# Optimization experiments

Measured on AMD Instinct MI355X. Metric: run time of the kernel, lower is better.

## Reference

```python
import jax, jax.numpy as jnp
import numpy as np
import math

D_MODEL = 512
N_HEADS = 2
B, S = 2, 1024
THRESHOLD = 0.5  # kwargs default 'sparsity_threshold'


def setup_inputs() -> dict:
    key = jax.random.key(0)
    ks = jax.random.split(key, 10)
    D, H = D_MODEL, D_MODEL // 4
    std = 0.02
    return {
        "x": jax.random.normal(ks[0], (B, S, D), jnp.float32),
        "Wq": jax.random.normal(ks[1], (D, D), jnp.float32) * std,
        "Wk": jax.random.normal(ks[2], (D, D), jnp.float32) * std,
        "Wv": jax.random.normal(ks[3], (D, D), jnp.float32) * std,
        "Wo": jax.random.normal(ks[4], (D, D), jnp.float32) * std,
        "bo": jnp.zeros((D,), jnp.float32),
        "W1": jax.random.normal(ks[5], (D, H), jnp.float32) * std,
        "b1": jnp.zeros((H,), jnp.float32),
        "W2": jax.random.normal(ks[6], (H, 1), jnp.float32) * std,
        "b2": jnp.zeros((1,), jnp.float32),
    }


def reference(x, Wq, Wk, Wv, Wo, bo, W1, b1, W2, b2):
    Bsz, Seq, D = x.shape
    Hn = N_HEADS
    dh = D // Hn

    def split_heads(t):
        return t.reshape(Bsz, Seq, Hn, dh).transpose(0, 2, 1, 3)  # [B,H,S,dh]

    q = split_heads(x @ Wq)
    k = split_heads(x @ Wk)
    v = split_heads(x @ Wv)

    scores = jnp.einsum("bhid,bhjd->bhij", q, k) / math.sqrt(dh)  # [B,H,S,S]

    # head-mean features for the pairwise sparsity predictor (n_heads==2 => 2*dh == D)
    q_mean = q.mean(axis=1)  # [B,S,dh]
    k_mean = k.mean(axis=1)  # [B,S,dh]
    # Linear1 of cat([q_mean_i, k_mean_j]) splits into two halves of W1
    a = q_mean @ W1[:dh]   # [B,S,Dh4]
    c = k_mean @ W1[dh:]   # [B,S,Dh4]
    hidden = jax.nn.relu(a[:, :, None, :] + c[:, None, :, :] + b1)  # [B,S,S,Dh4]
    connection_probs = jax.nn.sigmoid(jnp.squeeze(hidden @ W2, -1) + b2[0])  # [B,S,S]

    mask = connection_probs > THRESHOLD  # [B,S,S]
    scores = jnp.where(mask[:, None, :, :], scores, jnp.float32(-1e9))
    attn = jax.nn.softmax(scores, axis=-1)  # dropout inactive in eval

    out = jnp.einsum("bhij,bhjd->bhid", attn, v)  # [B,H,S,dh]
    out = out.transpose(0, 2, 1, 3).reshape(Bsz, Seq, D)
    out = out @ Wo + bo
    return out
```

## Files before the change

kernel.cpp:

```cpp
#include <hip/hip_runtime.h>


typedef unsigned short u16t;
typedef __bf16 bf16x8 __attribute__((ext_vector_type(8)));
typedef float f32x4 __attribute__((ext_vector_type(4)));

#define B_SZ 2
#define S_SZ 1024
#define D_SZ 512
#define DH 256
#define HH 128

static __device__ __forceinline__ u16t f2b(float f) {
    unsigned int u = __builtin_bit_cast(unsigned int, f);
    u += 0x7FFFu + ((u >> 16) & 1u);
    return (u16t)(u >> 16);
}

static __device__ __forceinline__ f32x4 mfma16(bf16x8 a, bf16x8 b, f32x4 c) {
    return __builtin_amdgcn_mfma_f32_16x16x32_bf16(a, b, c, 0, 0, 0);
}

static __device__ __forceinline__ void gload16(const void* g, void* l) {
    __builtin_amdgcn_global_load_lds(
        (const __attribute__((address_space(1))) void*)g,
        (__attribute__((address_space(3))) void*)l, 16, 0, 0);
}

__global__ __launch_bounds__(256) void k_prep(
    const float* __restrict__ x,
    const float* __restrict__ Wq, const float* __restrict__ Wk,
    const float* __restrict__ Wv, const float* __restrict__ Wo,
    const float* __restrict__ W1,
    u16t* __restrict__ xb, u16t* __restrict__ WT, float* __restrict__ Beff)
{
    __shared__ float smf[1088];
    int bidx = blockIdx.x;
    int t = threadIdx.x;
    if (bidx < 1024) {
        int idx = (bidx * 256 + t) * 4;
        float4 v = *(const float4*)(x + idx);
        u16t* o = xb + idx;
        o[0] = f2b(v.x); o[1] = f2b(v.y); o[2] = f2b(v.z); o[3] = f2b(v.w);
    } else if (bidx < 2048) {
        int t2 = bidx - 1024;
        int z = t2 >> 8, rem = t2 & 255;
        int n0 = (rem & 15) * 32, k0 = (rem >> 4) * 32;
        const float* W = z == 0 ? Wq : z == 1 ? Wk : z == 2 ? Wv : Wo;
        u16t* WTz = WT + (size_t)z * D_SZ * D_SZ;
        float (*tile)[33] = (float(*)[33])smf;
        int r = t >> 3, c4 = (t & 7) * 4;
        float4 v = *(const float4*)(W + (size_t)(k0 + r) * D_SZ + n0 + c4);
        tile[r][c4] = v.x; tile[r][c4 + 1] = v.y; tile[r][c4 + 2] = v.z; tile[r][c4 + 3] = v.w;
        __syncthreads();
        u16t o[4];
        o[0] = f2b(tile[c4][r]); o[1] = f2b(tile[c4 + 1][r]);
        o[2] = f2b(tile[c4 + 2][r]); o[3] = f2b(tile[c4 + 3][r]);
        *(ushort4*)(WTz + (size_t)(n0 + r) * D_SZ + k0 + c4) = *(ushort4*)o;
    } else {
        int k = bidx - 2048;
        float* wm0 = smf;
        float* wm1 = smf + 256;
        const float* wrq = Wq + (size_t)k * D_SZ;
        const float* wrk = Wk + (size_t)k * D_SZ;
        wm0[t & 255] = 0.5f * (wrq[t & 255] + wrq[(t & 255) + DH]);
        wm1[t & 255] = 0.5f * (wrk[t & 255] + wrk[(t & 255) + DH]);
        __syncthreads();
        int half = t >> 7, hcol = t & 127;
        const float* wm = half ? wm1 : wm0;
        const float* W1h = W1 + (half ? (size_t)DH * HH : 0);
        float s = 0.f;
        for (int d = 0; d < 256; ++d) s += wm[d] * W1h[(size_t)d * HH + hcol];
        Beff[(size_t)k * 256 + half * 128 + hcol] = s;
    }
}

template<int MF, int NF>
static __device__ __forceinline__ void gemm_db(
    const u16t* __restrict__ A, int lda, const u16t* __restrict__ B, int ldb,
    int K, int tid, u16t* Als, u16t* Bls, f32x4 acc[MF][NF])
{
    const int w = tid >> 6, lane = tid & 63;
    const int lr = lane & 15, kg = lane >> 4;
    const int srow = lane >> 3;
    const int scol = ((lane & 7) ^ srow) * 8;
    const int ABUF = MF * 4096;
    const int BBUF = NF * 1024;
    auto stage = [&](int bb, int k0) {
#pragma unroll
        for (int q = 0; q < MF * 2; ++q) {
            int ci = w * (MF * 2) + q;
            gload16(A + (size_t)(ci * 8 + srow) * lda + k0 + scol,
                    Als + bb * ABUF + ci * 512);
        }
#pragma unroll
        for (int q = 0; q < NF / 2; ++q) {
            int cj = w * (NF / 2) + q;
            gload16(B + (size_t)(cj * 8 + srow) * ldb + k0 + scol,
                    Bls + bb * BBUF + cj * 512);
        }
    };
    stage(0, 0);
    __syncthreads();
    const int nt = K / 64;
    for (int t = 0; t < nt; ++t) {
        int cur = t & 1;
        if (t + 1 < nt) stage(cur ^ 1, (t + 1) * 64);
        const u16t* Ab = Als + cur * ABUF;
        const u16t* Bb = Bls + cur * BBUF;
#pragma unroll
        for (int kk = 0; kk < 2; ++kk) {
            bf16x8 af[MF], bfr[NF];
#pragma unroll
            for (int fi = 0; fi < MF; ++fi) {
                int r = w * (MF * 16) + fi * 16 + lr;
                af[fi] = *(const bf16x8*)(&Ab[r * 64 + (((kk * 4 + kg) ^ (r & 7)) << 3)]);
            }
#pragma unroll
            for (int fj = 0; fj < NF; ++fj) {
                int r = fj * 16 + lr;
                bfr[fj] = *(const bf16x8*)(&Bb[r * 64 + (((kk * 4 + kg) ^ (r & 7)) << 3)]);
            }
#pragma unroll
            for (int fi = 0; fi < MF; ++fi)
#pragma unroll
                for (int fj = 0; fj < NF; ++fj)
                    acc[fi][fj] = mfma16(af[fi], bfr[fj], acc[fi][fj]);
        }
        __syncthreads();
    }
}


__global__ __launch_bounds__(256) void k_qkvac(
    const u16t* __restrict__ xb, const u16t* __restrict__ WT,
    const float* __restrict__ x, const float* __restrict__ Beff,
    const float* __restrict__ b1,
    u16t* __restrict__ qb, u16t* __restrict__ kb, u16t* __restrict__ vT,
    float* __restrict__ a, float* __restrict__ cc)
{
    __shared__ __align__(16) char sm[49152];
    int bid = blockIdx.x;
    int t = threadIdx.x;
    if (bid < 384) {
        u16t* Als = (u16t*)sm;
        u16t* Bls = (u16t*)(sm + 32768);
        int z = bid / 128, rem = bid & 127;
        int m0 = (rem >> 3) * 128, n0 = (rem & 7) * 64;
        const u16t* A = xb + (size_t)m0 * D_SZ;
        const u16t* Bt = WT + (size_t)z * D_SZ * D_SZ + (size_t)n0 * D_SZ;
        f32x4 acc[2][4] = {};
        gemm_db<2, 4>(A, D_SZ, Bt, D_SZ, D_SZ, t, Als, Bls, acc);
        int w = t >> 6, lane = t & 63, lr = lane & 15, kg = lane >> 4;
        if (z < 2) {
            u16t (*vls)[68] = (u16t(*)[68])sm;
            float scale = z == 0 ? 0.0625f : 1.0f;
#pragma unroll
            for (int fi = 0; fi < 2; ++fi)
#pragma unroll
                for (int fj = 0; fj < 4; ++fj)
#pragma unroll
                    for (int rr = 0; rr < 4; ++rr)
                        vls[w * 32 + fi * 16 + kg * 4 + rr][fj * 16 + lr]
                            = f2b(acc[fi][fj][rr] * scale);
            __syncthreads();
            u16t* dst = z == 0 ? qb : kb;
            int c8 = (t & 7) * 8, r0 = t >> 3;
#pragma unroll
            for (int p = 0; p < 4; ++p) {
                int r = r0 + p * 32;
                *(uint4*)(dst + (size_t)(m0 + r) * D_SZ + n0 + c8) = *(const uint4*)(&vls[r][c8]);
            }
        } else {
            u16t (*vls)[136] = (u16t(*)[136])sm;
#pragma unroll
            for (int fi = 0; fi < 2; ++fi)
#pragma unroll
                for (int fj = 0; fj < 4; ++fj)
#pragma unroll
                    for (int rr = 0; rr < 4; ++rr)
                        vls[fj * 16 + lr][w * 32 + fi * 16 + kg * 4 + rr] = f2b(acc[fi][fj][rr]);
            __syncthreads();
            int b = m0 >> 10, s0 = m0 & 1023;
            int cr = t >> 2, seg = t & 3;
            const u16t* srcp = &vls[cr][seg * 32];
            u16t* dstp = vT + (((size_t)(b * D_SZ + n0 + cr)) << 10) + s0 + seg * 32;
#pragma unroll
            for (int qq = 0; qq < 4; ++qq)
                *(uint4*)(dstp + qq * 8) = *(const uint4*)(srcp + qq * 8);
        }
    } else {
        float (*xs)[68] = (float(*)[68])sm;
        float (*bsT)[68] = (float(*)[68])(sm + 17408);
        int t2 = bid - 384;
        int r0 = (t2 & 31) * 64, n0 = (t2 >> 5) * 32;
        int ti = t >> 4, tj = t & 15;
        float acc[4][2] = {};
        for (int k0 = 0; k0 < 512; k0 += 64) {
            if (k0) __syncthreads();
#pragma unroll
            for (int p = 0; p < 4; ++p) {
                int idx = t + p * 256;
                int r = idx >> 4, c4 = (idx & 15) * 4;
                *(float4*)&xs[r][c4] = *(const float4*)(x + (size_t)(r0 + r) * D_SZ + k0 + c4);
            }
#pragma unroll
            for (int p = 0; p < 2; ++p) {
                int idx = t + p * 256;
                int k = idx >> 3, n4 = (idx & 7) * 4;
                float4 v = *(const float4*)(Beff + (size_t)(k0 + k) * 256 + n0 + n4);
                bsT[n4][k] = v.x; bsT[n4 + 1][k] = v.y; bsT[n4 + 2][k] = v.z; bsT[n4 + 3][k] = v.w;
            }
            __syncthreads();
#pragma unroll
            for (int kk = 0; kk < 16; ++kk) {
                float4 xv[4], bv[2];
#pragma unroll
                for (int ri = 0; ri < 4; ++ri) xv[ri] = *(const float4*)&xs[ti + 16 * ri][kk * 4];
#pragma unroll
                for (int rj = 0; rj < 2; ++rj) bv[rj] = *(const float4*)&bsT[tj + 16 * rj][kk * 4];
#pragma unroll
                for (int ri = 0; ri < 4; ++ri)
#pragma unroll
                    for (int rj = 0; rj < 2; ++rj)
                        acc[ri][rj] += xv[ri].x * bv[rj].x + xv[ri].y * bv[rj].y
                                     + xv[ri].z * bv[rj].z + xv[ri].w * bv[rj].w;
            }
        }
        bool isA = n0 < 128;
#pragma unroll
        for (int rj = 0; rj < 2; ++rj) {
            int col = n0 + tj + 16 * rj;
            float badd = isA ? b1[col] : 0.f;
#pragma unroll
            for (int ri = 0; ri < 4; ++ri) {
                int row = r0 + ti + 16 * ri;
                if (isA) a[(size_t)row * HH + col] = acc[ri][rj] + badd;
                else     cc[(size_t)row * HH + (col - 128)] = acc[ri][rj];
            }
        }
    }
}

__global__ __launch_bounds__(256) void k_scores(
    const u16t* __restrict__ qb, const u16t* __restrict__ kb,
    const float* __restrict__ a, const float* __restrict__ c,
    const float* __restrict__ W2, const float* __restrict__ b2,
    u16t* __restrict__ P, float* __restrict__ lpart)
{
    __shared__ __align__(16) char sm[38400];
    float (*at)[132] = (float(*)[132])sm;
    unsigned char (*msk)[64] = (unsigned char(*)[64])(sm + 33792);
    float* w2s = (float*)(sm + 37888);
    int b = blockIdx.z, mt = blockIdx.y, jb = blockIdx.x;
    int m0 = mt * 64, j0 = jb * 64;
    int t = threadIdx.x;
    if (t < 128) w2s[t] = W2[t];
#pragma unroll
    for (int p = 0; p < 8; ++p) {
        int idx = t + p * 256;
        int r = idx >> 5, c4 = (idx & 31) * 4;
        *(float4*)&at[r][c4] = *(const float4*)(a + ((size_t)(b * S_SZ + m0 + r)) * HH + c4);
    }
    float fb2 = b2[0];
    int ti = t >> 4, tj = t & 15;
    __syncthreads();
    {
        float accm[4][4];
#pragma unroll
        for (int ri = 0; ri < 4; ++ri)
#pragma unroll
            for (int rj = 0; rj < 4; ++rj) accm[ri][rj] = fb2;
        const float* crow[4];
#pragma unroll
        for (int rj = 0; rj < 4; ++rj)
            crow[rj] = c + (size_t)(b * S_SZ + j0 + tj + 16 * rj) * HH;
#pragma unroll 2
        for (int h4 = 0; h4 < 32; ++h4) {
            float4 wv = ((const float4*)w2s)[h4];
            float4 av[4], cv[4];
#pragma unroll
            for (int ri = 0; ri < 4; ++ri) av[ri] = *(const float4*)&at[ti + 16 * ri][h4 * 4];
#pragma unroll
            for (int rj = 0; rj < 4; ++rj) cv[rj] = ((const float4*)crow[rj])[h4];
#pragma unroll
            for (int ri = 0; ri < 4; ++ri)
#pragma unroll
                for (int rj = 0; rj < 4; ++rj) {
                    accm[ri][rj] += fmaxf(av[ri].x + cv[rj].x, 0.f) * wv.x;
                    accm[ri][rj] += fmaxf(av[ri].y + cv[rj].y, 0.f) * wv.y;
                    accm[ri][rj] += fmaxf(av[ri].z + cv[rj].z, 0.f) * wv.z;
                    accm[ri][rj] += fmaxf(av[ri].w + cv[rj].w, 0.f) * wv.w;
                }
        }
#pragma unroll
        for (int ri = 0; ri < 4; ++ri)
#pragma unroll
            for (int rj = 0; rj < 4; ++rj)
                msk[ti + 16 * ri][tj + 16 * rj] = accm[ri][rj] > 0.f ? 1 : 0;
    }
    __syncthreads();
    u16t* Als = (u16t*)sm;
    u16t* Bls = (u16t*)(sm + 16384);
    const u16t* A = qb + (size_t)(b * S_SZ + m0) * D_SZ;
    const u16t* B = kb + (size_t)(b * S_SZ + j0) * D_SZ;
    const int w = t >> 6, lane = t & 63, lr = lane & 15, kg = lane >> 4;
    const int srow = lane >> 3;
    const int scol = ((lane & 7) ^ srow) * 8;
    auto stage = [&](int bb, int k0) {
#pragma unroll
        for (int q = 0; q < 2; ++q) {
            int ci = w * 2 + q;
            gload16(A + (size_t)(ci * 8 + srow) * D_SZ + k0 + scol, Als + bb * 4096 + ci * 512);
            gload16(B + (size_t)(ci * 8 + srow) * D_SZ + k0 + scol, Bls + bb * 4096 + ci * 512);
        }
    };
    f32x4 acc0[4] = {}, acc1[4] = {};
    stage(0, 0);
    __syncthreads();
#pragma unroll
    for (int t8 = 0; t8 < 8; ++t8) {
        int cur = t8 & 1;
        if (t8 < 7) stage(cur ^ 1, (t8 + 1) * 64);
        const u16t* Ab = Als + cur * 4096;
        const u16t* Bb = Bls + cur * 4096;
#pragma unroll
        for (int kk = 0; kk < 2; ++kk) {
            int ra = w * 16 + lr;
            bf16x8 af = *(const bf16x8*)(&Ab[ra * 64 + (((kk * 4 + kg) ^ (ra & 7)) << 3)]);
            bf16x8 bfr[4];
#pragma unroll
            for (int fj = 0; fj < 4; ++fj) {
                int rb = fj * 16 + lr;
                bfr[fj] = *(const bf16x8*)(&Bb[rb * 64 + (((kk * 4 + kg) ^ (rb & 7)) << 3)]);
            }
            if (t8 < 4) {
#pragma unroll
                for (int fj = 0; fj < 4; ++fj) acc0[fj] = mfma16(af, bfr[fj], acc0[fj]);
            } else {
#pragma unroll
                for (int fj = 0; fj < 4; ++fj) acc1[fj] = mfma16(af, bfr[fj], acc1[fj]);
            }
        }
        __syncthreads();
    }
    u16t (*vls)[68] = (u16t(*)[68])sm;
#pragma unroll
    for (int h = 0; h < 2; ++h) {
#pragma unroll
        for (int rr = 0; rr < 4; ++rr) {
            int il = w * 16 + kg * 4 + rr;
            float rs = 0.f;
#pragma unroll
            for (int fj = 0; fj < 4; ++fj) {
                int jl = fj * 16 + lr;
                float s = h ? acc1[fj][rr] : acc0[fj][rr];
                float e = msk[il][jl] ? __expf(s) : 0.f;
                if (h) acc1[fj][rr] = e; else acc0[fj][rr] = e;
                rs += e;
            }
            rs += __shfl_xor(rs, 1); rs += __shfl_xor(rs, 2);
            rs += __shfl_xor(rs, 4); rs += __shfl_xor(rs, 8);
            if (lr == 0)
                lpart[((size_t)(jb * 4 + b * 2 + h) << 10) + m0 + il] = rs;
        }
#pragma unroll
        for (int fj = 0; fj < 4; ++fj)
#pragma unroll
            for (int rr = 0; rr < 4; ++rr)
                vls[w * 16 + kg * 4 + rr][fj * 16 + lr]
                    = f2b(h ? acc1[fj][rr] : acc0[fj][rr]);
        __syncthreads();
        int r = t >> 2, c16 = (t & 3) * 16;
        u16t* dstp = P + ((size_t)(b * 2 + h) << 20) + ((size_t)(m0 + r) << 10) + j0 + c16;
        *(uint4*)dstp = *(const uint4*)(&vls[r][c16]);
        *(uint4*)(dstp + 8) = *(const uint4*)(&vls[r][c16 + 8]);
        __syncthreads();
    }
}

__global__ __launch_bounds__(256) void k_pv(
    const u16t* __restrict__ P, const u16t* __restrict__ vT,
    const float* __restrict__ lpart, u16t* __restrict__ ao)
{
    __shared__ __align__(16) u16t sm[12288];
    __shared__ float invl[64];
    u16t* Als = sm;
    u16t* Bls = sm + 8192;
    int bh = blockIdx.z, b = bh >> 1, h = bh & 1;
    int m0 = blockIdx.y * 64, n0 = blockIdx.x * 32;
    int t = threadIdx.x;
    if (t < 64) {
        float l = 0.f;
        for (int jb = 0; jb < 16; ++jb)
            l += lpart[((size_t)(jb * 4 + bh) << 10) + m0 + t];
        invl[t] = l > 0.f ? 1.0f / l : 0.f;
    }
    const u16t* A = P + ((size_t)bh << 20) + (size_t)m0 * S_SZ;
    const u16t* Bt = vT + ((size_t)(b * D_SZ + h * DH + n0)) * S_SZ;
    f32x4 acc[1][2] = {};
    gemm_db<1, 2>(A, S_SZ, Bt, S_SZ, S_SZ, t, Als, Bls, acc);
    int w = t >> 6, lane = t & 63, lr = lane & 15, kg = lane >> 4;
    u16t (*ols)[40] = (u16t(*)[40])sm;
#pragma unroll
    for (int fj = 0; fj < 2; ++fj)
#pragma unroll
        for (int rr = 0; rr < 4; ++rr) {
            int rl = w * 16 + kg * 4 + rr;
            ols[rl][fj * 16 + lr] = f2b(acc[0][fj][rr] * invl[rl]);
        }
    __syncthreads();
    int r = t >> 2, c8 = (t & 3) * 8;
    *(uint4*)(ao + ((size_t)(b * S_SZ + m0 + r)) * D_SZ + h * DH + n0 + c8)
        = *(const uint4*)(&ols[r][c8]);
}

__global__ __launch_bounds__(256) void k_out(
    const u16t* __restrict__ ao, const u16t* __restrict__ WoT,
    const float* __restrict__ bo, float* __restrict__ out)
{
    __shared__ __align__(16) u16t sm[12288];
    u16t* Als = sm;
    u16t* Bls = sm + 8192;
    int m0 = blockIdx.y * 64, n0 = blockIdx.x * 32;
    const u16t* A = ao + (size_t)m0 * D_SZ;
    const u16t* Bt = WoT + (size_t)n0 * D_SZ;
    f32x4 acc[1][2] = {};
    gemm_db<1, 2>(A, D_SZ, Bt, D_SZ, D_SZ, threadIdx.x, Als, Bls, acc);
    int w = threadIdx.x >> 6, lane = threadIdx.x & 63, lr = lane & 15, kg = lane >> 4;
    float (*ols)[36] = (float(*)[36])sm;
#pragma unroll
    for (int fj = 0; fj < 2; ++fj)
#pragma unroll
        for (int rr = 0; rr < 4; ++rr) {
            int rl = w * 16 + kg * 4 + rr;
            ols[rl][fj * 16 + lr] = acc[0][fj][rr] + bo[n0 + fj * 16 + lr];
        }
    __syncthreads();
    int r0 = threadIdx.x >> 3, c4 = (threadIdx.x & 7) * 4;
#pragma unroll
    for (int p = 0; p < 2; ++p) {
        int r = r0 + p * 32;
        *(float4*)(out + (size_t)(m0 + r) * D_SZ + n0 + c4) = *(const float4*)(&ols[r][c4]);
    }
}

extern "C" void kernel_launch(void* const* d_in, const int* in_sizes, int n_in,
                              void* d_out, int out_size, void* d_ws, size_t ws_size,
                              hipStream_t stream)
{
    const float* x  = (const float*)d_in[0];
    const float* Wq = (const float*)d_in[1];
    const float* Wk = (const float*)d_in[2];
    const float* Wv = (const float*)d_in[3];
    const float* Wo = (const float*)d_in[4];
    const float* bo = (const float*)d_in[5];
    const float* W1 = (const float*)d_in[6];
    const float* b1 = (const float*)d_in[7];
    const float* W2 = (const float*)d_in[8];
    const float* b2 = (const float*)d_in[9];
    float* out = (float*)d_out;

    char* ws = (char*)d_ws;
    size_t off = 0;
    auto carve = [&](size_t bytes) { void* p = ws + off; off += (bytes + 255) & ~(size_t)255; return p; };
    u16t* xb   = (u16t*)carve((size_t)2048 * 512 * 2);
    u16t* WT   = (u16t*)carve((size_t)4 * 512 * 512 * 2);
    u16t* qb   = (u16t*)carve((size_t)2048 * 512 * 2);
    u16t* kb   = (u16t*)carve((size_t)2048 * 512 * 2);
    u16t* vT   = (u16t*)carve((size_t)2 * 512 * 1024 * 2);
    float* Beff = (float*)carve((size_t)512 * 256 * 4);
    float* a   = (float*)carve((size_t)2048 * 128 * 4);
    float* c   = (float*)carve((size_t)2048 * 128 * 4);
    u16t* P    = (u16t*)carve((size_t)4 * 1024 * 1024 * 2);
    float* lpart = (float*)carve((size_t)16 * 4 * 1024 * 4);
    u16t* ao   = (u16t*)carve((size_t)2048 * 512 * 2);
    (void)ws_size;

    k_prep<<<dim3(2560), dim3(256), 0, stream>>>(x, Wq, Wk, Wv, Wo, W1, xb, WT, Beff);
    k_qkvac<<<dim3(640), dim3(256), 0, stream>>>(xb, WT, x, Beff, b1, qb, kb, vT, a, c);
    k_scores<<<dim3(16, 16, 2), dim3(256), 0, stream>>>(qb, kb, a, c, W2, b2, P, lpart);
    k_pv<<<dim3(8, 16, 4), dim3(256), 0, stream>>>(P, vT, lpart, ao);
    k_out<<<dim3(16, 32), dim3(256), 0, stream>>>(ao, WT + (size_t)3 * 512 * 512, bo, out);
}
```

Measured before the change: 108.1 us.

## Interleave predictor MLP with QK^T MFMA staging to hide load latency

Merges the pairwise sparsity-predictor loop into the QK^T k-loop. Each of the eight k-steps issues async global-to-LDS loads for the Q/K tiles, then does four h4 steps of predictor arithmetic while those loads are in flight, and finally runs the MFMAs. The `a` rows are now read straight from global memory rather than staged through LDS, and the K-tile double buffer becomes a single buffer, which cuts LDS use from about 38KB to 21KB and may allow more blocks per CU. In exchange, `a` is read through global/cache per thread, and with a single buffer there is no cross-iteration prefetch, so each step waits on its own loads.

```diff
diff --git a/kernel.cpp b/kernel.cpp
--- a/kernel.cpp
+++ b/kernel.cpp
@@ -248,39 +248,52 @@
     const float* __restrict__ W2, const float* __restrict__ b2,
     u16t* __restrict__ P, float* __restrict__ lpart)
 {
-    __shared__ __align__(16) char sm[38400];
-    float (*at)[132] = (float(*)[132])sm;
-    unsigned char (*msk)[64] = (unsigned char(*)[64])(sm + 33792);
-    float* w2s = (float*)(sm + 37888);
+    __shared__ __align__(16) char sm[21504];
+    u16t* Als = (u16t*)sm;
+    u16t* Bls = (u16t*)(sm + 8192);
+    unsigned char (*msk)[64] = (unsigned char(*)[64])(sm + 16384);
+    float* w2s = (float*)(sm + 20480);
     int b = blockIdx.z, mt = blockIdx.y, jb = blockIdx.x;
     int m0 = mt * 64, j0 = jb * 64;
     int t = threadIdx.x;
     if (t < 128) w2s[t] = W2[t];
-#pragma unroll
-    for (int p = 0; p < 8; ++p) {
-        int idx = t + p * 256;
-        int r = idx >> 5, c4 = (idx & 31) * 4;
-        *(float4*)&at[r][c4] = *(const float4*)(a + ((size_t)(b * S_SZ + m0 + r)) * HH + c4);
-    }
     float fb2 = b2[0];
     int ti = t >> 4, tj = t & 15;
+    const int w = t >> 6, lane = t & 63, lr = lane & 15, kg = lane >> 4;
+    const int srow = lane >> 3;
+    const int scol = ((lane & 7) ^ srow) * 8;
+    const u16t* A = qb + (size_t)(b * S_SZ + m0) * D_SZ;
+    const u16t* B = kb + (size_t)(b * S_SZ + j0) * D_SZ;
+    const float* arow[4];
+    const float* crow[4];
+#pragma unroll
+    for (int ri = 0; ri < 4; ++ri)
+        arow[ri] = a + (size_t)(b * S_SZ + m0 + ti + 16 * ri) * HH;
+#pragma unroll
+    for (int rj = 0; rj < 4; ++rj)
+        crow[rj] = c + (size_t)(b * S_SZ + j0 + tj + 16 * rj) * HH;
+    float accm[4][4];
+#pragma unroll
+    for (int ri = 0; ri < 4; ++ri)
+#pragma unroll
+        for (int rj = 0; rj < 4; ++rj) accm[ri][rj] = fb2;
+    f32x4 acc0[4] = {}, acc1[4] = {};
     __syncthreads();
-    {
-        float accm[4][4];
-#pragma unroll
-        for (int ri = 0; ri < 4; ++ri)
-#pragma unroll
-            for (int rj = 0; rj < 4; ++rj) accm[ri][rj] = fb2;
-        const float* crow[4];
-#pragma unroll
-        for (int rj = 0; rj < 4; ++rj)
-            crow[rj] = c + (size_t)(b * S_SZ + j0 + tj + 16 * rj) * HH;
-#pragma unroll 2
-        for (int h4 = 0; h4 < 32; ++h4) {
+#pragma unroll
+    for (int t8 = 0; t8 < 8; ++t8) {
+#pragma unroll
+        for (int q = 0; q < 2; ++q) {
+            int ci = w * 2 + q;
+            gload16(A + (size_t)(ci * 8 + srow) * D_SZ + t8 * 64 + scol, Als + ci * 512);
+            gload16(B + (size_t)(ci * 8 + srow) * D_SZ + t8 * 64 + scol, Bls + ci * 512);
+        }
+#pragma unroll
+        for (int hh = 0; hh < 4; ++hh) {
+            int h4 = t8 * 4 + hh;
             float4 wv = ((const float4*)w2s)[h4];
             float4 av[4], cv[4];
 #pragma unroll
-            for (int ri = 0; ri < 4; ++ri) av[ri] = *(const float4*)&at[ti + 16 * ri][h4 * 4];
+            for (int ri = 0; ri < 4; ++ri) av[ri] = ((const float4*)arow[ri])[h4];
 #pragma unroll
             for (int rj = 0; rj < 4; ++rj) cv[rj] = ((const float4*)crow[rj])[h4];
 #pragma unroll
@@ -293,46 +306,16 @@
                     accm[ri][rj] += fmaxf(av[ri].w + cv[rj].w, 0.f) * wv.w;
                 }
         }
-#pragma unroll
-        for (int ri = 0; ri < 4; ++ri)
-#pragma unroll
-            for (int rj = 0; rj < 4; ++rj)
-                msk[ti + 16 * ri][tj + 16 * rj] = accm[ri][rj] > 0.f ? 1 : 0;
-    }
-    __syncthreads();
-    u16t* Als = (u16t*)sm;
-    u16t* Bls = (u16t*)(sm + 16384);
-    const u16t* A = qb + (size_t)(b * S_SZ + m0) * D_SZ;
-    const u16t* B = kb + (size_t)(b * S_SZ + j0) * D_SZ;
-    const int w = t >> 6, lane = t & 63, lr = lane & 15, kg = lane >> 4;
-    const int srow = lane >> 3;
-    const int scol = ((lane & 7) ^ srow) * 8;
-    auto stage = [&](int bb, int k0) {
-#pragma unroll
-        for (int q = 0; q < 2; ++q) {
-            int ci = w * 2 + q;
-            gload16(A + (size_t)(ci * 8 + srow) * D_SZ + k0 + scol, Als + bb * 4096 + ci * 512);
-            gload16(B + (size_t)(ci * 8 + srow) * D_SZ + k0 + scol, Bls + bb * 4096 + ci * 512);
-        }
-    };
-    f32x4 acc0[4] = {}, acc1[4] = {};
-    stage(0, 0);
-    __syncthreads();
-#pragma unroll
-    for (int t8 = 0; t8 < 8; ++t8) {
-        int cur = t8 & 1;
-        if (t8 < 7) stage(cur ^ 1, (t8 + 1) * 64);
-        const u16t* Ab = Als + cur * 4096;
-        const u16t* Bb = Bls + cur * 4096;
+        __syncthreads();
 #pragma unroll
         for (int kk = 0; kk < 2; ++kk) {
             int ra = w * 16 + lr;
-            bf16x8 af = *(const bf16x8*)(&Ab[ra * 64 + (((kk * 4 + kg) ^ (ra & 7)) << 3)]);
+            bf16x8 af = *(const bf16x8*)(&Als[ra * 64 + (((kk * 4 + kg) ^ (ra & 7)) << 3)]);
             bf16x8 bfr[4];
 #pragma unroll
             for (int fj = 0; fj < 4; ++fj) {
                 int rb = fj * 16 + lr;
-                bfr[fj] = *(const bf16x8*)(&Bb[rb * 64 + (((kk * 4 + kg) ^ (rb & 7)) << 3)]);
+                bfr[fj] = *(const bf16x8*)(&Bls[rb * 64 + (((kk * 4 + kg) ^ (rb & 7)) << 3)]);
             }
             if (t8 < 4) {
 #pragma unroll
@@ -344,6 +327,12 @@
         }
         __syncthreads();
     }
+#pragma unroll
+    for (int ri = 0; ri < 4; ++ri)
+#pragma unroll
+        for (int rj = 0; rj < 4; ++rj)
+            msk[ti + 16 * ri][tj + 16 * rj] = accm[ri][rj] > 0.f ? 1 : 0;
+    __syncthreads();
     u16t (*vls)[68] = (u16t(*)[68])sm;
 #pragma unroll
     for (int h = 0; h < 2; ++h) {
```

Result: slower. 142.9 us (+32.2%).
